# Kernel optimization log

Hardware: AMD Instinct MI355X
Metric: run time of the kernel (lower is better)

Reference implementation:

```python
import jax, jax.numpy as jnp
import numpy as np

B, D = 8192, 256


def setup_inputs() -> dict:
    key = jax.random.key(0)
    k1, k2 = jax.random.split(key)
    pred = jax.random.normal(k1, (B, D), dtype=jnp.float32)
    target = jax.random.normal(k2, (B, D), dtype=jnp.float32)
    noise_sigma = jnp.asarray(1.0, dtype=jnp.float32)  # learned scalar parameter
    return {"pred": pred, "target": target, "noise_sigma": noise_sigma}


def reference(pred, target, noise_sigma):
    # noise_var = sigma^2; MVN(pred_i, noise_var*I).log_prob(target_j)
    #   = -0.5*||target_j - pred_i||^2 / noise_var - 0.5*d*log(2*pi*noise_var)
    noise_var = noise_sigma ** 2
    d = pred.shape[-1]
    n = pred.shape[0]
    # pairwise squared distances via matmul (no [B,B,d] materialization)
    p2 = jnp.sum(pred * pred, axis=-1)      # [B]
    t2 = jnp.sum(target * target, axis=-1)  # [B]
    cross = pred @ target.T                 # [B, B]
    sqdist = p2[:, None] + t2[None, :] - 2.0 * cross  # [B, B]
    log_norm = 0.5 * d * jnp.log(2.0 * jnp.pi * noise_var)
    logits = -0.5 * sqdist / noise_var - log_norm  # [B, B]
    # cross_entropy(logits, arange(B)): mean over rows of -log_softmax diag
    logp = jax.nn.log_softmax(logits, axis=1)
    loss = -jnp.mean(jnp.diagonal(logp))
    # loss scaled by detached 2*noise_var
    return loss * jax.lax.stop_gradient(2.0 * noise_var)
```

## Files before the change

kernel.cpp:

```cpp
#include <hip/hip_runtime.h>
#include <stdint.h>

#define BATCH 8192
#define DIM 256
#define NSPLIT 16
#define BM 256
#define BN 32
#define COLS_PER_SPLIT (BATCH / NSPLIT)
#define NTILES (COLS_PER_SPLIT / BN)
#define LOG2E 1.4426950408889634f
#define LN2   0.6931471805599453f

typedef unsigned short ushort_t;
typedef float floatx4 __attribute__((ext_vector_type(4)));
typedef float floatx2 __attribute__((ext_vector_type(2)));
typedef int intx4 __attribute__((ext_vector_type(4)));
typedef int intx8 __attribute__((ext_vector_type(8)));

__device__ __forceinline__ float fast_exp2(float x) {
#if __has_builtin(__builtin_amdgcn_exp2f)
    return __builtin_amdgcn_exp2f(x);
#else
    return exp2f(x);
#endif
}

__global__ __launch_bounds__(256) void prep_kernel(
        const float* __restrict__ pred, const float* __restrict__ target,
        uint8_t* __restrict__ Ap, uint8_t* __restrict__ Bp,
        float* __restrict__ t2, float* __restrict__ diag) {
    __shared__ __align__(16) uint8_t ldsA[4096];
    __shared__ __align__(16) uint8_t ldsB[4096];
    const int t = threadIdx.x;
    const int r = t >> 4, c = t & 15;
    const int rt = blockIdx.x;
    const int row = rt * 16 + r;

    float dsum = 0.f, tsum = 0.f;
#pragma unroll
    for (int q = 0; q < 4; ++q) {
        const int k0 = q * 64 + c * 4;
        const float4 p4 = *(const float4*)(pred + (size_t)row * DIM + k0);
        const float4 t4 = *(const float4*)(target + (size_t)row * DIM + k0);
        dsum += p4.x * t4.x + p4.y * t4.y + p4.z * t4.z + p4.w * t4.w;
        tsum += t4.x * t4.x + t4.y * t4.y + t4.z * t4.z + t4.w * t4.w;
        const int kstep  = k0 >> 7;
        const int kgroup = (k0 >> 5) & 3;
        const int half   = (k0 >> 4) & 1;
        const int b      = k0 & 15;
        const int off = kstep * 2048 + half * 1024 + (kgroup * 16 + r) * 16 + b;
        int pp = __builtin_amdgcn_cvt_pk_fp8_f32(p4.x, p4.y, 0, false);
        pp     = __builtin_amdgcn_cvt_pk_fp8_f32(p4.z, p4.w, pp, true);
        int tt = __builtin_amdgcn_cvt_pk_fp8_f32(t4.x, t4.y, 0, false);
        tt     = __builtin_amdgcn_cvt_pk_fp8_f32(t4.z, t4.w, tt, true);
        *(int*)(ldsA + off) = pp;
        *(int*)(ldsB + off) = tt;
    }
#pragma unroll
    for (int mask = 1; mask < 16; mask <<= 1) {
        dsum += __shfl_xor(dsum, mask);
        tsum += __shfl_xor(tsum, mask);
    }
    if (c == 0) { diag[row] = dsum; t2[row] = tsum; }
    __syncthreads();

    const size_t base = (size_t)rt * 4096;
    const uint4 va = *(const uint4*)(ldsA + t * 16);
    const uint4 vb = *(const uint4*)(ldsB + t * 16);
    *(uint4*)(Ap + base + (size_t)t * 16) = va;
    *(uint4*)(Bp + base + (size_t)t * 16) = vb;
}

__global__ __launch_bounds__(256, 2) void main_kernel(
        const uint8_t* __restrict__ Ap, const uint8_t* __restrict__ Bp,
        const float* __restrict__ t2, const float* __restrict__ sigma,
        float2* __restrict__ partials) {
    __shared__ __align__(16) uint8_t ldsB[2][BN * DIM];

    const int lane   = threadIdx.x & 63;
    const int wave   = threadIdx.x >> 6;
    const int rowBlk = blockIdx.x;
    const int split  = blockIdx.y;

    const float sg = sigma[0];
    const float inv_nv = 1.0f / (sg * sg);
    const float c1 = LOG2E * inv_nv;
    const float c2 = -0.5f * c1;
    const float floor2 = -108.0f * c1;

    intx8 afrag[4][2];
#pragma unroll
    for (int mt = 0; mt < 4; ++mt) {
        const uint8_t* base = Ap + (size_t)(rowBlk * 16 + wave * 4 + mt) * 4096 + lane * 16;
#pragma unroll
        for (int ks = 0; ks < 2; ++ks) {
            const intx4 lo = *(const intx4*)(base + ks * 2048);
            const intx4 hi = *(const intx4*)(base + ks * 2048 + 1024);
            afrag[mt][ks] = (intx8){lo.x, lo.y, lo.z, lo.w, hi.x, hi.y, hi.z, hi.w};
        }
    }

    floatx2 m2[4][2], l2[4][2];
#pragma unroll
    for (int mt = 0; mt < 4; ++mt)
#pragma unroll
        for (int rp = 0; rp < 2; ++rp) {
            m2[mt][rp] = (floatx2){floor2, floor2};
            l2[mt][rp] = (floatx2){0.f, 0.f};
        }

    {
        const int j0 = split * COLS_PER_SPLIT;
        const char* gbase = (const char*)(Bp + (size_t)(j0 >> 4) * 4096);
#pragma unroll
        for (int q = 0; q < 2; ++q) {
            const int ch = wave * 2 + q;
            __builtin_amdgcn_global_load_lds(
                (const __attribute__((address_space(1))) void*)(gbase + ch * 1024 + (size_t)lane * 16),
                (__attribute__((address_space(3))) void*)((char*)ldsB[0] + ch * 1024),
                16, 0, 0);
        }
    }
    __syncthreads();

    for (int ct = 0; ct < NTILES; ++ct) {
        const uint8_t* cur = ldsB[ct & 1];
        const int j0 = split * COLS_PER_SPLIT + ct * BN;

        if (ct + 1 < NTILES) {
            const char* gbase = (const char*)(Bp + (size_t)((j0 + BN) >> 4) * 4096);
            char* lbase = (char*)ldsB[(ct + 1) & 1];
#pragma unroll
            for (int q = 0; q < 2; ++q) {
                const int ch = wave * 2 + q;
                __builtin_amdgcn_global_load_lds(
                    (const __attribute__((address_space(1))) void*)(gbase + ch * 1024 + (size_t)lane * 16),
                    (__attribute__((address_space(3))) void*)(lbase + ch * 1024),
                    16, 0, 0);
            }
        }

        float t2v0 = t2[j0 + (lane & 15)];
        float t2v1 = t2[j0 + 16 + (lane & 15)];

        floatx4 acc[4][2];
#pragma unroll
        for (int mt = 0; mt < 4; ++mt)
#pragma unroll
            for (int nt = 0; nt < 2; ++nt)
                acc[mt][nt] = (floatx4){0.f, 0.f, 0.f, 0.f};

#pragma unroll
        for (int ks = 0; ks < 2; ++ks) {
#pragma unroll
            for (int nt = 0; nt < 2; ++nt) {
                const uint8_t* bb = cur + nt * 4096 + ks * 2048 + lane * 16;
                const intx4 lo = *(const intx4*)(bb);
                const intx4 hi = *(const intx4*)(bb + 1024);
                const intx8 bfrag = (intx8){lo.x, lo.y, lo.z, lo.w, hi.x, hi.y, hi.z, hi.w};
#pragma unroll
                for (int mt = 0; mt < 4; ++mt) {
                    acc[mt][nt] = __builtin_amdgcn_mfma_scale_f32_16x16x128_f8f6f4(
                        afrag[mt][ks], bfrag, acc[mt][nt],
                        0, 0,
                        0, 127,
                        0, 127);
                }
            }
        }

        const float tvc0 = t2v0 * c2;
        const float tvc1 = t2v1 * c2;

        if (ct == 0) {
#pragma unroll
            for (int mt = 0; mt < 4; ++mt)
#pragma unroll
                for (int rp = 0; rp < 2; ++rp) {
                    const floatx2 v0 = (floatx2){acc[mt][0][2 * rp], acc[mt][0][2 * rp + 1]} * c1 + tvc0;
                    const floatx2 v1 = (floatx2){acc[mt][1][2 * rp], acc[mt][1][2 * rp + 1]} * c1 + tvc1;
                    floatx2 mm = __builtin_elementwise_max(v0, v1);
                    mm = __builtin_elementwise_max(mm, (floatx2){floor2, floor2});
                    m2[mt][rp] = mm;
                    floatx2 s;
                    s.x = fast_exp2(v0.x - mm.x) + fast_exp2(v1.x - mm.x);
                    s.y = fast_exp2(v0.y - mm.y) + fast_exp2(v1.y - mm.y);
                    l2[mt][rp] = s;
                }
        } else {
#pragma unroll
            for (int mt = 0; mt < 4; ++mt)
#pragma unroll
                for (int rp = 0; rp < 2; ++rp) {
                    const floatx2 mm = m2[mt][rp];
                    const floatx2 v0 = (floatx2){acc[mt][0][2 * rp], acc[mt][0][2 * rp + 1]} * c1 + (tvc0 - mm);
                    const floatx2 v1 = (floatx2){acc[mt][1][2 * rp], acc[mt][1][2 * rp + 1]} * c1 + (tvc1 - mm);
                    floatx2 s = l2[mt][rp];
                    s.x += fast_exp2(v0.x) + fast_exp2(v1.x);
                    s.y += fast_exp2(v0.y) + fast_exp2(v1.y);
                    l2[mt][rp] = s;
                }
        }

        __syncthreads();
    }

#pragma unroll
    for (int mt = 0; mt < 4; ++mt)
#pragma unroll
        for (int rp = 0; rp < 2; ++rp)
#pragma unroll
            for (int z = 0; z < 2; ++z) {
                float m = m2[mt][rp][z];
                float l = l2[mt][rp][z];
#pragma unroll
                for (int mask = 1; mask < 16; mask <<= 1) {
                    const float mo = __shfl_xor(m, mask);
                    const float lo = __shfl_xor(l, mask);
                    const float mn = fmaxf(m, mo);
                    l = l * fast_exp2(m - mn) + lo * fast_exp2(mo - mn);
                    m = mn;
                }
                if ((lane & 15) == 0) {
                    const int r  = rp * 2 + z;
                    const int rw = rowBlk * BM + wave * 64 + mt * 16 + (lane >> 4) * 4 + r;
                    partials[(size_t)split * BATCH + rw] = make_float2(m, l);
                }
            }
}

__global__ __launch_bounds__(256) void finish1_kernel(
        const float2* __restrict__ partials, const float* __restrict__ t2,
        const float* __restrict__ diag, const float* __restrict__ sigma,
        float* __restrict__ bsum) {
    __shared__ float red[256];
    const int tid = threadIdx.x;
    const int row = blockIdx.x * 256 + tid;
    const float sg = sigma[0];
    const float inv_nv = 1.0f / (sg * sg);

    float2 p[NSPLIT];
    float m = -__builtin_inff();
#pragma unroll
    for (int s = 0; s < NSPLIT; ++s) {
        p[s] = partials[(size_t)s * BATCH + row];
        m = fmaxf(m, p[s].x);
    }
    float L = 0.0f;
#pragma unroll
    for (int s = 0; s < NSPLIT; ++s)
        L += p[s].y * fast_exp2(p[s].x - m);
    const float lse_nat = LN2 * (m + __log2f(L));
    const float d = (diag[row] - 0.5f * t2[row]) * inv_nv;
    red[tid] = lse_nat - d;
    __syncthreads();
    for (int s = 128; s > 0; s >>= 1) {
        if (tid < s) red[tid] += red[tid + s];
        __syncthreads();
    }
    if (tid == 0) bsum[blockIdx.x] = red[0];
}

__global__ __launch_bounds__(64) void finish2_kernel(
        const float* __restrict__ bsum, const float* __restrict__ sigma,
        float* __restrict__ out) {
    const int tid = threadIdx.x;
    float v = (tid < 32) ? bsum[tid] : 0.0f;
#pragma unroll
    for (int mask = 32; mask > 0; mask >>= 1)
        v += __shfl_xor(v, mask);
    if (tid == 0) {
        const float nv = sigma[0] * sigma[0];
        out[0] = 2.0f * nv * v / (float)BATCH;
    }
}

extern "C" void kernel_launch(void* const* d_in, const int* in_sizes, int n_in,
                              void* d_out, int out_size, void* d_ws, size_t ws_size,
                              hipStream_t stream) {
    const float* pred   = (const float*)d_in[0];
    const float* target = (const float*)d_in[1];
    const float* sigma  = (const float*)d_in[2];
    float* out = (float*)d_out;

    char* ws = (char*)d_ws;
    uint8_t* Ap   = (uint8_t*)(ws);
    uint8_t* Bp   = (uint8_t*)(ws + (size_t)BATCH * DIM);
    float* t2     = (float*)(ws + (size_t)BATCH * DIM * 4);
    float* diag   = (float*)(ws + (size_t)BATCH * DIM * 4 + BATCH * 4);
    float2* parts = (float2*)(ws + (size_t)BATCH * DIM * 4 + (size_t)BATCH * 8);
    float* bsum   = (float*)(ws + (size_t)BATCH * DIM * 4 + (size_t)BATCH * 8
                             + (size_t)NSPLIT * BATCH * 8);

    prep_kernel<<<BATCH / 16, 256, 0, stream>>>(pred, target, Ap, Bp, t2, diag);
    main_kernel<<<dim3(BATCH / BM, NSPLIT), 256, 0, stream>>>(Ap, Bp, t2, sigma, parts);
    finish1_kernel<<<BATCH / 256, 256, 0, stream>>>(parts, t2, diag, sigma, bsum);
    finish2_kernel<<<1, 64, 0, stream>>>(bsum, sigma, out);
}
```

Before: 96.25 us.

## Fuse finish kernels into main via last-block atomics and widen column tile

Removes the two finish kernel launches. The last split block for each row block now merges the partial logsumexp values, and a global atomic counter lets the final block write the loss. The column tile also grows from 32 to 64, which gives more MFMA work per LDS tile and per sync and halves the loop trip count. In exchange it raises register pressure (16 accumulators) and LDS use, and the atomic float add makes the summation order nondeterministic.

```diff
diff --git a/kernel.cpp b/kernel.cpp
--- a/kernel.cpp
+++ b/kernel.cpp
@@ -5,13 +5,13 @@
 #define DIM 256
 #define NSPLIT 16
 #define BM 256
-#define BN 32
+#define BN 64
 #define COLS_PER_SPLIT (BATCH / NSPLIT)
 #define NTILES (COLS_PER_SPLIT / BN)
+#define NROWBLK (BATCH / BM)
 #define LOG2E 1.4426950408889634f
 #define LN2   0.6931471805599453f
 
-typedef unsigned short ushort_t;
 typedef float floatx4 __attribute__((ext_vector_type(4)));
 typedef float floatx2 __attribute__((ext_vector_type(2)));
 typedef int intx4 __attribute__((ext_vector_type(4)));
@@ -28,13 +28,21 @@
 __global__ __launch_bounds__(256) void prep_kernel(
         const float* __restrict__ pred, const float* __restrict__ target,
         uint8_t* __restrict__ Ap, uint8_t* __restrict__ Bp,
-        float* __restrict__ t2, float* __restrict__ diag) {
+        float* __restrict__ t2, float* __restrict__ diag,
+        int* __restrict__ cnt, int* __restrict__ cnt2,
+        float* __restrict__ gacc) {
     __shared__ __align__(16) uint8_t ldsA[4096];
     __shared__ __align__(16) uint8_t ldsB[4096];
     const int t = threadIdx.x;
     const int r = t >> 4, c = t & 15;
     const int rt = blockIdx.x;
     const int row = rt * 16 + r;
+
+    if (rt == 0) {
+        if (t < NROWBLK) cnt[t] = 0;
+        if (t == NROWBLK) *cnt2 = 0;
+        if (t == NROWBLK + 1) *gacc = 0.0f;
+    }
 
     float dsum = 0.f, tsum = 0.f;
 #pragma unroll
@@ -73,8 +81,10 @@
 
 __global__ __launch_bounds__(256, 2) void main_kernel(
         const uint8_t* __restrict__ Ap, const uint8_t* __restrict__ Bp,
-        const float* __restrict__ t2, const float* __restrict__ sigma,
-        float2* __restrict__ partials) {
+        const float* __restrict__ t2, const float* __restrict__ diag,
+        const float* __restrict__ sigma, float2* __restrict__ partials,
+        int* __restrict__ cnt, int* __restrict__ cnt2,
+        float* __restrict__ gacc, float* __restrict__ out) {
     __shared__ __align__(16) uint8_t ldsB[2][BN * DIM];
 
     const int lane   = threadIdx.x & 63;
@@ -83,7 +93,8 @@
     const int split  = blockIdx.y;
 
     const float sg = sigma[0];
-    const float inv_nv = 1.0f / (sg * sg);
+    const float nv = sg * sg;
+    const float inv_nv = 1.0f / nv;
     const float c1 = LOG2E * inv_nv;
     const float c2 = -0.5f * c1;
     const float floor2 = -108.0f * c1;
@@ -113,8 +124,8 @@
         const int j0 = split * COLS_PER_SPLIT;
         const char* gbase = (const char*)(Bp + (size_t)(j0 >> 4) * 4096);
 #pragma unroll
-        for (int q = 0; q < 2; ++q) {
-            const int ch = wave * 2 + q;
+        for (int q = 0; q < 4; ++q) {
+            const int ch = wave * 4 + q;
             __builtin_amdgcn_global_load_lds(
                 (const __attribute__((address_space(1))) void*)(gbase + ch * 1024 + (size_t)lane * 16),
                 (__attribute__((address_space(3))) void*)((char*)ldsB[0] + ch * 1024),
@@ -131,8 +142,8 @@
             const char* gbase = (const char*)(Bp + (size_t)((j0 + BN) >> 4) * 4096);
             char* lbase = (char*)ldsB[(ct + 1) & 1];
 #pragma unroll
-            for (int q = 0; q < 2; ++q) {
-                const int ch = wave * 2 + q;
+            for (int q = 0; q < 4; ++q) {
+                const int ch = wave * 4 + q;
                 __builtin_amdgcn_global_load_lds(
                     (const __attribute__((address_space(1))) void*)(gbase + ch * 1024 + (size_t)lane * 16),
                     (__attribute__((address_space(3))) void*)(lbase + ch * 1024),
@@ -140,20 +151,22 @@
             }
         }
 
-        float t2v0 = t2[j0 + (lane & 15)];
-        float t2v1 = t2[j0 + 16 + (lane & 15)];
-
-        floatx4 acc[4][2];
+        float t2v[4];
+#pragma unroll
+        for (int nt = 0; nt < 4; ++nt)
+            t2v[nt] = t2[j0 + nt * 16 + (lane & 15)];
+
+        floatx4 acc[4][4];
 #pragma unroll
         for (int mt = 0; mt < 4; ++mt)
 #pragma unroll
-            for (int nt = 0; nt < 2; ++nt)
+            for (int nt = 0; nt < 4; ++nt)
                 acc[mt][nt] = (floatx4){0.f, 0.f, 0.f, 0.f};
 
 #pragma unroll
         for (int ks = 0; ks < 2; ++ks) {
 #pragma unroll
-            for (int nt = 0; nt < 2; ++nt) {
+            for (int nt = 0; nt < 4; ++nt) {
                 const uint8_t* bb = cur + nt * 4096 + ks * 2048 + lane * 16;
                 const intx4 lo = *(const intx4*)(bb);
                 const intx4 hi = *(const intx4*)(bb + 1024);
@@ -169,22 +182,30 @@
             }
         }
 
-        const float tvc0 = t2v0 * c2;
-        const float tvc1 = t2v1 * c2;
+        float tvc[4];
+#pragma unroll
+        for (int nt = 0; nt < 4; ++nt) tvc[nt] = t2v[nt] * c2;
 
         if (ct == 0) {
 #pragma unroll
             for (int mt = 0; mt < 4; ++mt)
 #pragma unroll
                 for (int rp = 0; rp < 2; ++rp) {
-                    const floatx2 v0 = (floatx2){acc[mt][0][2 * rp], acc[mt][0][2 * rp + 1]} * c1 + tvc0;
-                    const floatx2 v1 = (floatx2){acc[mt][1][2 * rp], acc[mt][1][2 * rp + 1]} * c1 + tvc1;
-                    floatx2 mm = __builtin_elementwise_max(v0, v1);
+                    floatx2 v[4];
+#pragma unroll
+                    for (int nt = 0; nt < 4; ++nt)
+                        v[nt] = (floatx2){acc[mt][nt][2 * rp], acc[mt][nt][2 * rp + 1]} * c1 + tvc[nt];
+                    floatx2 mm = __builtin_elementwise_max(
+                        __builtin_elementwise_max(v[0], v[1]),
+                        __builtin_elementwise_max(v[2], v[3]));
                     mm = __builtin_elementwise_max(mm, (floatx2){floor2, floor2});
                     m2[mt][rp] = mm;
-                    floatx2 s;
-                    s.x = fast_exp2(v0.x - mm.x) + fast_exp2(v1.x - mm.x);
-                    s.y = fast_exp2(v0.y - mm.y) + fast_exp2(v1.y - mm.y);
+                    floatx2 s = (floatx2){0.f, 0.f};
+#pragma unroll
+                    for (int nt = 0; nt < 4; ++nt) {
+                        s.x += fast_exp2(v[nt].x - mm.x);
+                        s.y += fast_exp2(v[nt].y - mm.y);
+                    }
                     l2[mt][rp] = s;
                 }
         } else {
@@ -193,11 +214,14 @@
 #pragma unroll
                 for (int rp = 0; rp < 2; ++rp) {
                     const floatx2 mm = m2[mt][rp];
-                    const floatx2 v0 = (floatx2){acc[mt][0][2 * rp], acc[mt][0][2 * rp + 1]} * c1 + (tvc0 - mm);
-                    const floatx2 v1 = (floatx2){acc[mt][1][2 * rp], acc[mt][1][2 * rp + 1]} * c1 + (tvc1 - mm);
                     floatx2 s = l2[mt][rp];
-                    s.x += fast_exp2(v0.x) + fast_exp2(v1.x);
-                    s.y += fast_exp2(v0.y) + fast_exp2(v1.y);
+#pragma unroll
+                    for (int nt = 0; nt < 4; ++nt) {
+                        const floatx2 v = (floatx2){acc[mt][nt][2 * rp], acc[mt][nt][2 * rp + 1]} * c1
+                                          + (tvc[nt] - mm);
+                        s.x += fast_exp2(v.x);
+                        s.y += fast_exp2(v.y);
+                    }
                     l2[mt][rp] = s;
                 }
         }
@@ -227,18 +251,17 @@
                     partials[(size_t)split * BATCH + rw] = make_float2(m, l);
                 }
             }
-}
-
-__global__ __launch_bounds__(256) void finish1_kernel(
-        const float2* __restrict__ partials, const float* __restrict__ t2,
-        const float* __restrict__ diag, const float* __restrict__ sigma,
-        float* __restrict__ bsum) {
-    __shared__ float red[256];
+
+    __threadfence();
+    __shared__ int isLast;
+    if (threadIdx.x == 0)
+        isLast = (atomicAdd(&cnt[rowBlk], 1) == NSPLIT - 1);
+    __syncthreads();
+    if (!isLast) return;
+
+    __threadfence();
     const int tid = threadIdx.x;
-    const int row = blockIdx.x * 256 + tid;
-    const float sg = sigma[0];
-    const float inv_nv = 1.0f / (sg * sg);
-
+    const int row = rowBlk * BM + tid;
     float2 p[NSPLIT];
     float m = -__builtin_inff();
 #pragma unroll
@@ -252,26 +275,21 @@
         L += p[s].y * fast_exp2(p[s].x - m);
     const float lse_nat = LN2 * (m + __log2f(L));
     const float d = (diag[row] - 0.5f * t2[row]) * inv_nv;
+
+    float* red = (float*)ldsB;
     red[tid] = lse_nat - d;
     __syncthreads();
     for (int s = 128; s > 0; s >>= 1) {
         if (tid < s) red[tid] += red[tid + s];
         __syncthreads();
     }
-    if (tid == 0) bsum[blockIdx.x] = red[0];
-}
-
-__global__ __launch_bounds__(64) void finish2_kernel(
-        const float* __restrict__ bsum, const float* __restrict__ sigma,
-        float* __restrict__ out) {
-    const int tid = threadIdx.x;
-    float v = (tid < 32) ? bsum[tid] : 0.0f;
-#pragma unroll
-    for (int mask = 32; mask > 0; mask >>= 1)
-        v += __shfl_xor(v, mask);
     if (tid == 0) {
-        const float nv = sigma[0] * sigma[0];
-        out[0] = 2.0f * nv * v / (float)BATCH;
+        atomicAdd(gacc, red[0]);
+        __threadfence();
+        if (atomicAdd(cnt2, 1) == NROWBLK - 1) {
+            const float tot = atomicAdd(gacc, 0.0f);
+            out[0] = 2.0f * nv * tot / (float)BATCH;
+        }
     }
 }
 
@@ -289,11 +307,15 @@
     float* t2     = (float*)(ws + (size_t)BATCH * DIM * 4);
     float* diag   = (float*)(ws + (size_t)BATCH * DIM * 4 + BATCH * 4);
     float2* parts = (float2*)(ws + (size_t)BATCH * DIM * 4 + (size_t)BATCH * 8);
-    float* bsum   = (float*)(ws + (size_t)BATCH * DIM * 4 + (size_t)BATCH * 8
-                             + (size_t)NSPLIT * BATCH * 8);
-
-    prep_kernel<<<BATCH / 16, 256, 0, stream>>>(pred, target, Ap, Bp, t2, diag);
-    main_kernel<<<dim3(BATCH / BM, NSPLIT), 256, 0, stream>>>(Ap, Bp, t2, sigma, parts);
-    finish1_kernel<<<BATCH / 256, 256, 0, stream>>>(parts, t2, diag, sigma, bsum);
-    finish2_kernel<<<1, 64, 0, stream>>>(bsum, sigma, out);
+    char* tail    = ws + (size_t)BATCH * DIM * 4 + (size_t)BATCH * 8
+                       + (size_t)NSPLIT * BATCH * 8;
+    int* cnt      = (int*)tail;
+    int* cnt2     = (int*)(tail + 128);
+    float* gacc   = (float*)(tail + 192);
+
+    prep_kernel<<<BATCH / 16, 256, 0, stream>>>(pred, target, Ap, Bp, t2, diag,
+                                                cnt, cnt2, gacc);
+    main_kernel<<<dim3(NROWBLK, NSPLIT), 256, 0, stream>>>(Ap, Bp, t2, diag,
+                                                           sigma, parts,
+                                                           cnt, cnt2, gacc, out);
 }
```

Result: slower. 137.1 us (+42.4%).
